# Optimization experiments

Hardware: AMD Instinct MI355X
Metric: run time of the kernel (lower is better)

Reference implementation:

```python
import jax, jax.numpy as jnp
import numpy as np

LN_EPS = 1e-12  # BERT default layer_norm_eps


def setup_inputs() -> dict:
    key = jax.random.key(0)
    ks = jax.random.split(key, 8)
    B, S, H, I, E = 4, 2048, 1024, 4096, 8
    sH = 1.0 / np.sqrt(H)
    sI = 1.0 / np.sqrt(I)
    return {
        "hidden_states": jax.random.normal(ks[0], (B, S, H), dtype=jnp.float32),
        "Wr": jax.random.uniform(ks[1], (E, H), jnp.float32, -sH, sH),      # router (no bias)
        "W1": jax.random.uniform(ks[2], (E, H, I), jnp.float32, -sH, sH),   # per-expert BertIntermediate
        "b1": jax.random.uniform(ks[3], (E, I), jnp.float32, -sH, sH),
        "Wo": jax.random.uniform(ks[4], (I, H), jnp.float32, -sI, sI),      # shared BertOutput dense
        "bo": jax.random.uniform(ks[5], (H,), jnp.float32, -sI, sI),
        "gamma": jnp.ones((H,), jnp.float32),
        "beta": jnp.zeros((H,), jnp.float32),
    }


def reference(hidden_states, Wr, W1, b1, Wo, bo, gamma, beta):
    B, S, H = hidden_states.shape
    E = Wr.shape[0]
    x = hidden_states.reshape(-1, H)                      # [N, H]
    router_logits = x @ Wr.T                              # [N, E]
    # top-1 expert per token (router probs are NOT used to scale outputs in the original)
    expert_idx = jnp.argmax(jax.nn.softmax(router_logits, axis=-1), axis=-1)  # [N]
    # dispatch == per-token expert FFN; accumulate masked per-expert outputs
    inter = jnp.zeros((x.shape[0], W1.shape[2]), dtype=x.dtype)  # [N, I]
    for e in range(E):  # fixed small expert count
        mask = (expert_idx == e)[:, None].astype(x.dtype)
        inter = inter + mask * jax.nn.gelu(x @ W1[e] + b1[e], approximate=False)
    # shared BertOutput: dense -> (dropout off) -> residual -> LayerNorm
    y = inter @ Wo + bo + x                               # [N, H]
    mu = jnp.mean(y, axis=-1, keepdims=True)
    var = jnp.mean(jnp.square(y - mu), axis=-1, keepdims=True)
    out = (y - mu) * jax.lax.rsqrt(var + LN_EPS) * gamma + beta
    return out.reshape(B, S, H)
```

## Files before the change

### kernel.cpp

```cpp
#include <hip/hip_runtime.h>
#include <hip/hip_bf16.h>
#include <math.h>

#define NTOK 8192
#define HD 1024
#define ID 4096
#define NE 8
#define MAXTILES 72
#define SORTT 512
#define TPT (NTOK / SORTT)

typedef __attribute__((ext_vector_type(8))) short short8;
typedef __attribute__((ext_vector_type(8))) unsigned short ushort8;
typedef __attribute__((ext_vector_type(4))) float floatx4;

__device__ __forceinline__ unsigned short f2bf(float f) {
  unsigned int u = __float_as_uint(f);
  return (unsigned short)((u + 0x7fffu + ((u >> 16) & 1u)) >> 16);
}

__device__ __forceinline__ void async_ld16(const void* g, void* l) {
  __builtin_amdgcn_global_load_lds(
      (const __attribute__((address_space(1))) unsigned int*)g,
      (__attribute__((address_space(3))) unsigned int*)l,
      16, 0, 0);
}


__global__ void transpose_cast_kernel(const float* __restrict__ src,
                                      unsigned short* __restrict__ dst, int R, int C) {
  size_t bo = (size_t)blockIdx.z * R * C;
  src += bo; dst += bo;
  __shared__ float t[64][65];
  int c0 = blockIdx.x * 64, r0 = blockIdx.y * 64;
  int tid = threadIdx.x;
  int rr = tid >> 4, c4 = (tid & 15) * 4;
#pragma unroll
  for (int q = 0; q < 4; q++) {
    int r = rr + q * 16;
    float4 v = *(const float4*)(src + (size_t)(r0 + r) * C + c0 + c4);
    t[r][c4] = v.x; t[r][c4 + 1] = v.y; t[r][c4 + 2] = v.z; t[r][c4 + 3] = v.w;
  }
  __syncthreads();
  int r8 = (tid & 7) * 8;
#pragma unroll
  for (int q = 0; q < 2; q++) {
    int cc = (tid >> 3) + q * 32;
    ushort8 o;
#pragma unroll
    for (int i = 0; i < 8; i++) o[i] = f2bf(t[r8 + i][cc]);
    *(ushort8*)(dst + (size_t)(c0 + cc) * R + r0 + r8) = o;
  }
}

__global__ void router_kernel(const float* __restrict__ x, const float* __restrict__ wr,
                              int* __restrict__ eidx, unsigned short* __restrict__ xb) {
  int wave = threadIdx.x >> 6, lane = threadIdx.x & 63;
  int n = blockIdx.x * 4 + wave;
  const float* xr = x + (size_t)n * HD;
  unsigned short* xbr = xb + (size_t)n * HD;
  double acc[NE];
#pragma unroll
  for (int e = 0; e < NE; e++) acc[e] = 0.0;
#pragma unroll
  for (int v = 0; v < 4; v++) {
    int h = (lane + v * 64) * 4;
    float4 xv = *(const float4*)(xr + h);
    ushort4 o;
    o.x = f2bf(xv.x); o.y = f2bf(xv.y); o.z = f2bf(xv.z); o.w = f2bf(xv.w);
    *(ushort4*)(xbr + h) = o;
#pragma unroll
    for (int e = 0; e < NE; e++) {
      float4 wv = *(const float4*)(wr + e * HD + h);
      acc[e] += (double)xv.x * wv.x + (double)xv.y * wv.y +
                (double)xv.z * wv.z + (double)xv.w * wv.w;
    }
  }
#pragma unroll
  for (int m = 32; m >= 1; m >>= 1) {
#pragma unroll
    for (int e = 0; e < NE; e++) acc[e] += __shfl_xor(acc[e], m, 64);
  }
  if (lane == 0) {
    int best = 0; double bv = acc[0];
#pragma unroll
    for (int e = 1; e < NE; e++) if (acc[e] > bv) { bv = acc[e]; best = e; }
    eidx[n] = best;
  }
}

__global__ __launch_bounds__(SORTT) void sort_kernel(
    const int* __restrict__ eidx, int* __restrict__ ntiles, int* __restrict__ tile_e,
    int* __restrict__ tile_base, int* __restrict__ tile_len, int* __restrict__ perm) {
  __shared__ int h[NE][SORTT];
  __shared__ int off_sh[NE];
  __shared__ int tot[NE];
  int t = threadIdx.x;
  int wave = t >> 6, lane = t & 63;
  const int base = t * TPT;

  int4 e0 = *(const int4*)(eidx + base);
  int4 e1 = *(const int4*)(eidx + base + 4);
  int4 e2 = *(const int4*)(eidx + base + 8);
  int4 e3 = *(const int4*)(eidx + base + 12);
  int ex[TPT] = {e0.x, e0.y, e0.z, e0.w, e1.x, e1.y, e1.z, e1.w,
                 e2.x, e2.y, e2.z, e2.w, e3.x, e3.y, e3.z, e3.w};
  int cnt0 = 0, cnt1 = 0, cnt2 = 0, cnt3 = 0, cnt4 = 0, cnt5 = 0, cnt6 = 0, cnt7 = 0;
#pragma unroll
  for (int i = 0; i < TPT; i++) {
    int e = ex[i];
    cnt0 += (e == 0); cnt1 += (e == 1); cnt2 += (e == 2); cnt3 += (e == 3);
    cnt4 += (e == 4); cnt5 += (e == 5); cnt6 += (e == 6); cnt7 += (e == 7);
  }
  h[0][t] = cnt0; h[1][t] = cnt1; h[2][t] = cnt2; h[3][t] = cnt3;
  h[4][t] = cnt4; h[5][t] = cnt5; h[6][t] = cnt6; h[7][t] = cnt7;
  __syncthreads();

  {
    int e = wave;
    int v[8], s = 0;
#pragma unroll
    for (int i = 0; i < 8; i++) { v[i] = h[e][lane * 8 + i]; s += v[i]; }
    int inc = s;
#pragma unroll
    for (int d = 1; d < 64; d <<= 1) {
      int o = __shfl_up(inc, d, 64);
      if (lane >= d) inc += o;
    }
    int exc = inc - s;
#pragma unroll
    for (int i = 0; i < 8; i++) { h[e][lane * 8 + i] = exc; exc += v[i]; }
    if (lane == 63) tot[e] = inc;
  }
  __syncthreads();

  if (t == 0) {
    int s = 0, tt = 0;
    for (int e = 0; e < NE; e++) {
      off_sh[e] = s;
      int c = tot[e];
      for (int b = 0; b < c; b += 128) {
        tile_e[tt] = e;
        tile_base[tt] = s + b;
        tile_len[tt] = (c - b < 128) ? (c - b) : 128;
        tt++;
      }
      s += c;
    }
    *ntiles = tt;
  }
  __syncthreads();

  int c0c = off_sh[0] + h[0][t], c1c = off_sh[1] + h[1][t];
  int c2c = off_sh[2] + h[2][t], c3c = off_sh[3] + h[3][t];
  int c4c = off_sh[4] + h[4][t], c5c = off_sh[5] + h[5][t];
  int c6c = off_sh[6] + h[6][t], c7c = off_sh[7] + h[7][t];
#pragma unroll
  for (int i = 0; i < TPT; i++) {
    int e = ex[i];
    int pos = c0c;
    pos = (e == 1) ? c1c : pos; pos = (e == 2) ? c2c : pos;
    pos = (e == 3) ? c3c : pos; pos = (e == 4) ? c4c : pos;
    pos = (e == 5) ? c5c : pos; pos = (e == 6) ? c6c : pos;
    pos = (e == 7) ? c7c : pos;
    perm[pos] = base + i;
    c0c += (e == 0); c1c += (e == 1); c2c += (e == 2); c3c += (e == 3);
    c4c += (e == 4); c5c += (e == 5); c6c += (e == 6); c7c += (e == 7);
  }
}


__global__ __launch_bounds__(256, 2) void ffn1_kernel(
    const unsigned short* __restrict__ xb, const unsigned short* __restrict__ w1t,
    const float* __restrict__ b1, const int* __restrict__ perm,
    const int* __restrict__ ntiles, const int* __restrict__ tile_e,
    const int* __restrict__ tile_base, const int* __restrict__ tile_len,
    unsigned short* __restrict__ interb) {
  int t = blockIdx.y;
  if (t >= *ntiles) return;
  int e = tile_e[t], base = tile_base[t], len = tile_len[t];
  int nb = blockIdx.x * 128;

  __shared__ unsigned short lA[128 * 64];
  __shared__ unsigned short lB[128 * 64];

  int tid = threadIdx.x;
  int wave = tid >> 6, lane = tid & 63;
  int lr = lane >> 3;
  int chunk = (lane & 7) ^ lr;

  const unsigned short* gA[4];
  const unsigned short* gB[4];
#pragma unroll
  for (int q = 0; q < 4; q++) {
    int c = wave * 4 + q;
    int tr = c * 8 + lr;
    int token = perm[base + (tr < len ? tr : len - 1)];
    gA[q] = xb + (size_t)token * HD + chunk * 8;
    int nr = nb + c * 8 + lr;
    gB[q] = w1t + ((size_t)e * ID + nr) * HD + chunk * 8;
  }

  floatx4 acc[4][4];
#pragma unroll
  for (int i = 0; i < 4; i++)
#pragma unroll
    for (int j = 0; j < 4; j++) acc[i][j] = (floatx4){0.f, 0.f, 0.f, 0.f};

  int wm = (wave >> 1) * 64, wn = (wave & 1) * 64;
  int c15 = lane & 15, q4 = lane >> 4;

  for (int ko = 0; ko < HD / 64; ko++) {
#pragma unroll
    for (int q = 0; q < 4; q++) {
      int c = wave * 4 + q;
      async_ld16(gA[q] + ko * 64, &lA[c * 512]);
      async_ld16(gB[q] + ko * 64, &lB[c * 512]);
    }
    __syncthreads();
#pragma unroll
    for (int kk = 0; kk < 2; kk++) {
      short8 af[4], bfr[4];
#pragma unroll
      for (int i = 0; i < 4; i++) {
        int m = wm + i * 16 + c15;
        int sa = (kk * 4 + q4) ^ (m & 7);
        af[i] = *(const short8*)&lA[m * 64 + sa * 8];
        int n = wn + i * 16 + c15;
        int sb = (kk * 4 + q4) ^ (n & 7);
        bfr[i] = *(const short8*)&lB[n * 64 + sb * 8];
      }
#pragma unroll
      for (int i = 0; i < 4; i++)
#pragma unroll
        for (int j = 0; j < 4; j++)
          acc[i][j] = __builtin_amdgcn_mfma_f32_16x16x32_bf16(af[i], bfr[j], acc[i][j], 0, 0, 0);
    }
    __syncthreads();
  }

#pragma unroll
  for (int i = 0; i < 4; i++) {
#pragma unroll
    for (int r = 0; r < 4; r++) {
      int tr = wm + i * 16 + q4 * 4 + r;
      if (tr >= len) continue;
      int token = perm[base + tr];
#pragma unroll
      for (int j = 0; j < 4; j++) {
        int col = nb + wn + j * 16 + c15;
        float v = acc[i][j][r] + b1[e * ID + col];
        v = 0.5f * v * (1.0f + erff(v * 0.70710678118654752f));
        interb[(size_t)token * ID + col] = f2bf(v);
      }
    }
  }
}

__global__ __launch_bounds__(256, 2) void ffn2_kernel(
    const unsigned short* __restrict__ interb, const unsigned short* __restrict__ wot,
    const float* __restrict__ bo, const float* __restrict__ x, float* __restrict__ y) {
  int tm = blockIdx.y;
  int nb = blockIdx.x * 128;

  __shared__ unsigned short lA[128 * 64];
  __shared__ unsigned short lB[128 * 64];

  int tid = threadIdx.x;
  int wave = tid >> 6, lane = tid & 63;
  int lr = lane >> 3;
  int chunk = (lane & 7) ^ lr;

  const unsigned short* gA[4];
  const unsigned short* gB[4];
#pragma unroll
  for (int q = 0; q < 4; q++) {
    int c = wave * 4 + q;
    int row = tm * 128 + c * 8 + lr;
    gA[q] = interb + (size_t)row * ID + chunk * 8;
    int nr = nb + c * 8 + lr;
    gB[q] = wot + (size_t)nr * ID + chunk * 8;
  }

  floatx4 acc[4][4];
#pragma unroll
  for (int i = 0; i < 4; i++)
#pragma unroll
    for (int j = 0; j < 4; j++) acc[i][j] = (floatx4){0.f, 0.f, 0.f, 0.f};

  int wm = (wave >> 1) * 64, wn = (wave & 1) * 64;
  int c15 = lane & 15, q4 = lane >> 4;

  for (int ko = 0; ko < ID / 64; ko++) {
#pragma unroll
    for (int q = 0; q < 4; q++) {
      int c = wave * 4 + q;
      async_ld16(gA[q] + ko * 64, &lA[c * 512]);
      async_ld16(gB[q] + ko * 64, &lB[c * 512]);
    }
    __syncthreads();
#pragma unroll
    for (int kk = 0; kk < 2; kk++) {
      short8 af[4], bfr[4];
#pragma unroll
      for (int i = 0; i < 4; i++) {
        int m = wm + i * 16 + c15;
        int sa = (kk * 4 + q4) ^ (m & 7);
        af[i] = *(const short8*)&lA[m * 64 + sa * 8];
        int n = wn + i * 16 + c15;
        int sb = (kk * 4 + q4) ^ (n & 7);
        bfr[i] = *(const short8*)&lB[n * 64 + sb * 8];
      }
#pragma unroll
      for (int i = 0; i < 4; i++)
#pragma unroll
        for (int j = 0; j < 4; j++)
          acc[i][j] = __builtin_amdgcn_mfma_f32_16x16x32_bf16(af[i], bfr[j], acc[i][j], 0, 0, 0);
    }
    __syncthreads();
  }

#pragma unroll
  for (int i = 0; i < 4; i++) {
#pragma unroll
    for (int r = 0; r < 4; r++) {
      int row = tm * 128 + wm + i * 16 + q4 * 4 + r;
#pragma unroll
      for (int j = 0; j < 4; j++) {
        int col = nb + wn + j * 16 + c15;
        float v = acc[i][j][r] + bo[col] + x[(size_t)row * HD + col];
        y[(size_t)row * HD + col] = v;
      }
    }
  }
}

__global__ void ln_kernel(float* __restrict__ y, const float* __restrict__ gamma,
                          const float* __restrict__ beta) {
  int row = blockIdx.x, t = threadIdx.x;
  int lane = t & 63, wave = t >> 6;
  float* yr = y + (size_t)row * HD;
  float4 v = *(const float4*)(yr + t * 4);
  float s = v.x + v.y + v.z + v.w;
  float ss = v.x * v.x + v.y * v.y + v.z * v.z + v.w * v.w;
#pragma unroll
  for (int m = 32; m >= 1; m >>= 1) {
    s += __shfl_xor(s, m, 64);
    ss += __shfl_xor(ss, m, 64);
  }
  __shared__ float sred[4], ssred[4];
  if (lane == 0) { sred[wave] = s; ssred[wave] = ss; }
  __syncthreads();
  s = sred[0] + sred[1] + sred[2] + sred[3];
  ss = ssred[0] + ssred[1] + ssred[2] + ssred[3];
  float mu = s * (1.0f / HD);
  float var = ss * (1.0f / HD) - mu * mu;
  float rs = rsqrtf(var + 1e-12f);
  float4 g = *(const float4*)(gamma + t * 4);
  float4 b = *(const float4*)(beta + t * 4);
  float4 o;
  o.x = (v.x - mu) * rs * g.x + b.x;
  o.y = (v.y - mu) * rs * g.y + b.y;
  o.z = (v.z - mu) * rs * g.z + b.z;
  o.w = (v.w - mu) * rs * g.w + b.w;
  *(float4*)(yr + t * 4) = o;
}


extern "C" void kernel_launch(void* const* d_in, const int* in_sizes, int n_in,
                              void* d_out, int out_size, void* d_ws, size_t ws_size,
                              hipStream_t stream) {
  const float* x     = (const float*)d_in[0];
  const float* wr    = (const float*)d_in[1];
  const float* w1    = (const float*)d_in[2];
  const float* b1    = (const float*)d_in[3];
  const float* wo    = (const float*)d_in[4];
  const float* bo    = (const float*)d_in[5];
  const float* gamma = (const float*)d_in[6];
  const float* beta  = (const float*)d_in[7];
  float* out = (float*)d_out;

  char* p = (char*)d_ws;
  unsigned short* w1t = (unsigned short*)p; p += (size_t)NE * ID * HD * 2;
  unsigned short* wot = (unsigned short*)p; p += (size_t)HD * ID * 2;
  unsigned short* xb  = (unsigned short*)p; p += (size_t)NTOK * HD * 2;
  unsigned short* interb = (unsigned short*)p; p += (size_t)NTOK * ID * 2;
  int* eidx = (int*)p; p += (size_t)NTOK * 4;
  int* perm = (int*)p; p += (size_t)NTOK * 4;
  int* ints = (int*)p;
  int* ntiles    = ints;
  int* tile_e    = ints + 8;
  int* tile_base = ints + 80;
  int* tile_len  = ints + 152;

  router_kernel<<<NTOK / 4, 256, 0, stream>>>(x, wr, eidx, xb);
  transpose_cast_kernel<<<dim3(ID / 64, HD / 64, NE), 256, 0, stream>>>(w1, w1t, HD, ID);
  transpose_cast_kernel<<<dim3(HD / 64, ID / 64, 1), 256, 0, stream>>>(wo, wot, ID, HD);
  sort_kernel<<<1, SORTT, 0, stream>>>(eidx, ntiles, tile_e, tile_base, tile_len, perm);
  ffn1_kernel<<<dim3(ID / 128, MAXTILES), 256, 0, stream>>>(
      xb, w1t, b1, perm, ntiles, tile_e, tile_base, tile_len, interb);
  ffn2_kernel<<<dim3(HD / 128, NTOK / 128), 256, 0, stream>>>(interb, wot, bo, x, out);
  ln_kernel<<<NTOK, 256, 0, stream>>>(out, gamma, beta);
}
```

Before: 500.2 us.

## Double-buffer LDS tiles in both expert GEMM kernels to overlap loads

Both the expert FFN1 and shared FFN2 GEMM kernels get two LDS buffers per operand. The tile for the next K step is issued with async global-to-LDS loads before the MFMA work on the current tile. This removes the pre-compute barrier that left matrix cores idle during each global load. In exchange, LDS use per block doubles to 64 KB, which could limit occupancy, and correctness relies on the end-of-iteration barrier waiting for the outstanding async loads.

```diff
diff --git a/kernel.cpp b/kernel.cpp
--- a/kernel.cpp
+++ b/kernel.cpp
@@ -170,6 +170,8 @@
 }
 
 
+#define LBUF (128 * 64)
+
 __global__ __launch_bounds__(256, 2) void ffn1_kernel(
     const unsigned short* __restrict__ xb, const unsigned short* __restrict__ w1t,
     const float* __restrict__ b1, const int* __restrict__ perm,
@@ -181,8 +183,8 @@
   int e = tile_e[t], base = tile_base[t], len = tile_len[t];
   int nb = blockIdx.x * 128;
 
-  __shared__ unsigned short lA[128 * 64];
-  __shared__ unsigned short lB[128 * 64];
+  __shared__ unsigned short lA[2 * LBUF];
+  __shared__ unsigned short lB[2 * LBUF];
 
   int tid = threadIdx.x;
   int wave = tid >> 6, lane = tid & 63;
@@ -210,14 +212,26 @@
   int wm = (wave >> 1) * 64, wn = (wave & 1) * 64;
   int c15 = lane & 15, q4 = lane >> 4;
 
-  for (int ko = 0; ko < HD / 64; ko++) {
-#pragma unroll
-    for (int q = 0; q < 4; q++) {
-      int c = wave * 4 + q;
-      async_ld16(gA[q] + ko * 64, &lA[c * 512]);
-      async_ld16(gB[q] + ko * 64, &lB[c * 512]);
-    }
-    __syncthreads();
+  const int NK = HD / 64;
+#pragma unroll
+  for (int q = 0; q < 4; q++) {
+    int c = wave * 4 + q;
+    async_ld16(gA[q], &lA[c * 512]);
+    async_ld16(gB[q], &lB[c * 512]);
+  }
+  __syncthreads();
+
+  for (int ko = 0; ko < NK; ko++) {
+    int cur = (ko & 1) * LBUF;
+    int nxt = (cur ^ LBUF);
+    if (ko + 1 < NK) {
+#pragma unroll
+      for (int q = 0; q < 4; q++) {
+        int c = wave * 4 + q;
+        async_ld16(gA[q] + (ko + 1) * 64, &lA[nxt + c * 512]);
+        async_ld16(gB[q] + (ko + 1) * 64, &lB[nxt + c * 512]);
+      }
+    }
 #pragma unroll
     for (int kk = 0; kk < 2; kk++) {
       short8 af[4], bfr[4];
@@ -225,10 +239,10 @@
       for (int i = 0; i < 4; i++) {
         int m = wm + i * 16 + c15;
         int sa = (kk * 4 + q4) ^ (m & 7);
-        af[i] = *(const short8*)&lA[m * 64 + sa * 8];
+        af[i] = *(const short8*)&lA[cur + m * 64 + sa * 8];
         int n = wn + i * 16 + c15;
         int sb = (kk * 4 + q4) ^ (n & 7);
-        bfr[i] = *(const short8*)&lB[n * 64 + sb * 8];
+        bfr[i] = *(const short8*)&lB[cur + n * 64 + sb * 8];
       }
 #pragma unroll
       for (int i = 0; i < 4; i++)
@@ -263,8 +277,8 @@
   int tm = blockIdx.y;
   int nb = blockIdx.x * 128;
 
-  __shared__ unsigned short lA[128 * 64];
-  __shared__ unsigned short lB[128 * 64];
+  __shared__ unsigned short lA[2 * LBUF];
+  __shared__ unsigned short lB[2 * LBUF];
 
   int tid = threadIdx.x;
   int wave = tid >> 6, lane = tid & 63;
@@ -291,14 +305,26 @@
   int wm = (wave >> 1) * 64, wn = (wave & 1) * 64;
   int c15 = lane & 15, q4 = lane >> 4;
 
-  for (int ko = 0; ko < ID / 64; ko++) {
-#pragma unroll
-    for (int q = 0; q < 4; q++) {
-      int c = wave * 4 + q;
-      async_ld16(gA[q] + ko * 64, &lA[c * 512]);
-      async_ld16(gB[q] + ko * 64, &lB[c * 512]);
-    }
-    __syncthreads();
+  const int NK = ID / 64;
+#pragma unroll
+  for (int q = 0; q < 4; q++) {
+    int c = wave * 4 + q;
+    async_ld16(gA[q], &lA[c * 512]);
+    async_ld16(gB[q], &lB[c * 512]);
+  }
+  __syncthreads();
+
+  for (int ko = 0; ko < NK; ko++) {
+    int cur = (ko & 1) * LBUF;
+    int nxt = (cur ^ LBUF);
+    if (ko + 1 < NK) {
+#pragma unroll
+      for (int q = 0; q < 4; q++) {
+        int c = wave * 4 + q;
+        async_ld16(gA[q] + (ko + 1) * 64, &lA[nxt + c * 512]);
+        async_ld16(gB[q] + (ko + 1) * 64, &lB[nxt + c * 512]);
+      }
+    }
 #pragma unroll
     for (int kk = 0; kk < 2; kk++) {
       short8 af[4], bfr[4];
@@ -306,10 +332,10 @@
       for (int i = 0; i < 4; i++) {
         int m = wm + i * 16 + c15;
         int sa = (kk * 4 + q4) ^ (m & 7);
-        af[i] = *(const short8*)&lA[m * 64 + sa * 8];
+        af[i] = *(const short8*)&lA[cur + m * 64 + sa * 8];
         int n = wn + i * 16 + c15;
         int sb = (kk * 4 + q4) ^ (n & 7);
-        bfr[i] = *(const short8*)&lB[n * 64 + sb * 8];
+        bfr[i] = *(const short8*)&lB[cur + n * 64 + sb * 8];
       }
 #pragma unroll
       for (int i = 0; i < 4; i++)
```

Result: slower. 547.3 us (+9.4%).

## Use 256x256 tiles with double-buffered 8-phase async pipeline in FFN GEMMs

Applied to the files above, without the earlier changes.

Both expert and output GEMMs move from 128x128 tiles with 4 waves and a single LDS buffer to 256x256 tiles with 8 waves. Global-to-LDS async loads are double-buffered and interleaved across eight MFMA phases using explicit vmcnt waits, barriers and setprio. Expert tiles in the sort kernel grow to 256 tokens, with MAXTILES reduced to 40. The aim is to hide load latency and raise arithmetic intensity. The cost is 128KB of LDS per block, which may limit occupancy, and more padding waste on partial expert tiles.

```diff
diff --git a/kernel.cpp b/kernel.cpp
--- a/kernel.cpp
+++ b/kernel.cpp
@@ -6,7 +6,7 @@
 #define HD 1024
 #define ID 4096
 #define NE 8
-#define MAXTILES 72
+#define MAXTILES 40
 #define SORTT 512
 #define TPT (NTOK / SORTT)
 
@@ -139,10 +139,10 @@
     for (int e = 0; e < NE; e++) {
       off_sh[e] = s;
       int c = tot[e];
-      for (int b = 0; b < c; b += 128) {
+      for (int b = 0; b < c; b += 256) {
         tile_e[tt] = e;
         tile_base[tt] = s + b;
-        tile_len[tt] = (c - b < 128) ? (c - b) : 128;
+        tile_len[tt] = (c - b < 256) ? (c - b) : 256;
         tt++;
       }
       s += c;
@@ -170,7 +170,91 @@
 }
 
 
-__global__ __launch_bounds__(256, 2) void ffn1_kernel(
+#define VMC6() asm volatile("s_waitcnt vmcnt(6)" ::: "memory")
+#define VMC0() asm volatile("s_waitcnt vmcnt(0)" ::: "memory")
+#define NOPS ((void)0)
+
+#define SA8(BUF, kt, q) \
+  async_ld16(gAq[q] + (size_t)(kt) * 64, lA + ((BUF) * 16384 + ((q) * 64 + wave * 8) * 64))
+#define SB8(BUF, kt, q) \
+  async_ld16(gBq[q] + (size_t)(kt) * 64, lB + ((BUF) * 16384 + ((q) * 64 + wave * 8) * 64))
+
+#define MF4(AV, KK, I)                                                                       \
+  acc[I][0] = __builtin_amdgcn_mfma_f32_16x16x32_bf16(AV, bf[0][KK], acc[I][0], 0, 0, 0);    \
+  acc[I][1] = __builtin_amdgcn_mfma_f32_16x16x32_bf16(AV, bf[1][KK], acc[I][1], 0, 0, 0);    \
+  acc[I][2] = __builtin_amdgcn_mfma_f32_16x16x32_bf16(AV, bf[2][KK], acc[I][2], 0, 0, 0);    \
+  acc[I][3] = __builtin_amdgcn_mfma_f32_16x16x32_bf16(AV, bf[3][KK], acc[I][3], 0, 0, 0);
+
+#define PH8(BT, I, STG, TAIL)                                                  \
+  {                                                                            \
+    short8 a0k0 = *(const short8*)(lA + (BT) * 16384 + aoff[I] + sx0);         \
+    short8 a0k1 = *(const short8*)(lA + (BT) * 16384 + aoff[I] + sx1);         \
+    short8 a1k0 = *(const short8*)(lA + (BT) * 16384 + aoff[(I) + 1] + sx0);   \
+    short8 a1k1 = *(const short8*)(lA + (BT) * 16384 + aoff[(I) + 1] + sx1);   \
+    STG;                                                                       \
+    __builtin_amdgcn_s_barrier();                                              \
+    __builtin_amdgcn_s_setprio(1);                                             \
+    MF4(a0k0, 0, I) MF4(a0k1, 1, I)                                            \
+    MF4(a1k0, 0, (I) + 1) MF4(a1k1, 1, (I) + 1)                                \
+    __builtin_amdgcn_s_setprio(0);                                             \
+    TAIL;                                                                      \
+    __builtin_amdgcn_s_barrier();                                              \
+  }
+
+#define LOADB8(BT)                                                             \
+  bf[0][0] = *(const short8*)(lB + (BT) * 16384 + boff[0] + sx0);              \
+  bf[0][1] = *(const short8*)(lB + (BT) * 16384 + boff[0] + sx1);              \
+  bf[1][0] = *(const short8*)(lB + (BT) * 16384 + boff[1] + sx0);              \
+  bf[1][1] = *(const short8*)(lB + (BT) * 16384 + boff[1] + sx1);              \
+  bf[2][0] = *(const short8*)(lB + (BT) * 16384 + boff[2] + sx0);              \
+  bf[2][1] = *(const short8*)(lB + (BT) * 16384 + boff[2] + sx1);              \
+  bf[3][0] = *(const short8*)(lB + (BT) * 16384 + boff[3] + sx0);              \
+  bf[3][1] = *(const short8*)(lB + (BT) * 16384 + boff[3] + sx1);
+
+template <int NK>
+__device__ __forceinline__ void gemm8phase(const unsigned short* const* gAq,
+                                           const unsigned short* const* gBq,
+                                           unsigned short* lA, unsigned short* lB,
+                                           int wave, int lane, floatx4 (&acc)[8][4]) {
+  int c15 = lane & 15, q4 = lane >> 4, c7 = c15 & 7;
+  int wm = wave >> 2, wn = wave & 3;
+  int sx0 = (q4 ^ c7) * 8;
+  int sx1 = ((4 + q4) ^ c7) * 8;
+  int aoff[8], boff[4];
+#pragma unroll
+  for (int i = 0; i < 8; i++) aoff[i] = (wm * 128 + i * 16 + c15) * 64;
+#pragma unroll
+  for (int j = 0; j < 4; j++) boff[j] = (wn * 64 + j * 16 + c15) * 64;
+
+  SB8(0, 0, 0); SB8(0, 0, 1); SB8(0, 0, 2); SB8(0, 0, 3);
+  SA8(0, 0, 0); SA8(0, 0, 2); SA8(0, 0, 1); SA8(0, 0, 3);
+  SB8(1, 1, 0); SB8(1, 1, 1); SB8(1, 1, 2); SB8(1, 1, 3);
+  SA8(1, 1, 0); SA8(1, 1, 2);
+  VMC6();
+  __builtin_amdgcn_s_barrier();
+
+  short8 bf[4][2];
+#pragma unroll 1
+  for (int u = 0; u < NK / 2; ++u) {
+    int kt0 = 2 * u;
+    bool last = (u == NK / 2 - 1);
+    LOADB8(0)
+    PH8(0, 0, SA8(1, kt0 + 1, 1); SA8(1, kt0 + 1, 3), NOPS)
+    PH8(0, 2, if (!last) { SB8(0, kt0 + 2, 0); SB8(0, kt0 + 2, 1); }, NOPS)
+    PH8(0, 4, if (!last) { SB8(0, kt0 + 2, 2); SB8(0, kt0 + 2, 3); }, NOPS)
+    PH8(0, 6, if (!last) { SA8(0, kt0 + 2, 0); SA8(0, kt0 + 2, 2); },
+        if (last) VMC0(); else VMC6())
+    LOADB8(1)
+    PH8(1, 0, if (!last) { SA8(0, kt0 + 2, 1); SA8(0, kt0 + 2, 3); }, NOPS)
+    PH8(1, 2, if (!last) { SB8(1, kt0 + 3, 0); SB8(1, kt0 + 3, 1); }, NOPS)
+    PH8(1, 4, if (!last) { SB8(1, kt0 + 3, 2); SB8(1, kt0 + 3, 3); }, NOPS)
+    PH8(1, 6, if (!last) { SA8(1, kt0 + 3, 0); SA8(1, kt0 + 3, 2); },
+        if (!last) VMC6())
+  }
+}
+
+
+__global__ __launch_bounds__(512, 2) void ffn1_kernel(
     const unsigned short* __restrict__ xb, const unsigned short* __restrict__ w1t,
     const float* __restrict__ b1, const int* __restrict__ perm,
     const int* __restrict__ ntiles, const int* __restrict__ tile_e,
@@ -179,76 +263,46 @@
   int t = blockIdx.y;
   if (t >= *ntiles) return;
   int e = tile_e[t], base = tile_base[t], len = tile_len[t];
-  int nb = blockIdx.x * 128;
-
-  __shared__ unsigned short lA[128 * 64];
-  __shared__ unsigned short lB[128 * 64];
+  int nb = blockIdx.x * 256;
+
+  __shared__ unsigned short lA[2 * 16384];
+  __shared__ unsigned short lB[2 * 16384];
 
   int tid = threadIdx.x;
   int wave = tid >> 6, lane = tid & 63;
-  int lr = lane >> 3;
-  int chunk = (lane & 7) ^ lr;
-
-  const unsigned short* gA[4];
-  const unsigned short* gB[4];
+  int lr = lane >> 3, l7 = lane & 7;
+  int chunk = l7 ^ lr;
+
+  const unsigned short* gAq[4];
+  const unsigned short* gBq[4];
 #pragma unroll
   for (int q = 0; q < 4; q++) {
-    int c = wave * 4 + q;
-    int tr = c * 8 + lr;
-    int token = perm[base + (tr < len ? tr : len - 1)];
-    gA[q] = xb + (size_t)token * HD + chunk * 8;
-    int nr = nb + c * 8 + lr;
-    gB[q] = w1t + ((size_t)e * ID + nr) * HD + chunk * 8;
-  }
-
-  floatx4 acc[4][4];
-#pragma unroll
-  for (int i = 0; i < 4; i++)
+    int rr = q * 64 + wave * 8 + lr;
+    int token = perm[base + (rr < len ? rr : len - 1)];
+    gAq[q] = xb + (size_t)token * HD + chunk * 8;
+    gBq[q] = w1t + ((size_t)e * ID + nb + rr) * HD + chunk * 8;
+  }
+
+  floatx4 acc[8][4];
+#pragma unroll
+  for (int i = 0; i < 8; i++)
 #pragma unroll
     for (int j = 0; j < 4; j++) acc[i][j] = (floatx4){0.f, 0.f, 0.f, 0.f};
 
-  int wm = (wave >> 1) * 64, wn = (wave & 1) * 64;
+  gemm8phase<HD / 64>(gAq, gBq, lA, lB, wave, lane, acc);
+
   int c15 = lane & 15, q4 = lane >> 4;
-
-  for (int ko = 0; ko < HD / 64; ko++) {
-#pragma unroll
-    for (int q = 0; q < 4; q++) {
-      int c = wave * 4 + q;
-      async_ld16(gA[q] + ko * 64, &lA[c * 512]);
-      async_ld16(gB[q] + ko * 64, &lB[c * 512]);
-    }
-    __syncthreads();
-#pragma unroll
-    for (int kk = 0; kk < 2; kk++) {
-      short8 af[4], bfr[4];
-#pragma unroll
-      for (int i = 0; i < 4; i++) {
-        int m = wm + i * 16 + c15;
-        int sa = (kk * 4 + q4) ^ (m & 7);
-        af[i] = *(const short8*)&lA[m * 64 + sa * 8];
-        int n = wn + i * 16 + c15;
-        int sb = (kk * 4 + q4) ^ (n & 7);
-        bfr[i] = *(const short8*)&lB[n * 64 + sb * 8];
-      }
-#pragma unroll
-      for (int i = 0; i < 4; i++)
-#pragma unroll
-        for (int j = 0; j < 4; j++)
-          acc[i][j] = __builtin_amdgcn_mfma_f32_16x16x32_bf16(af[i], bfr[j], acc[i][j], 0, 0, 0);
-    }
-    __syncthreads();
-  }
-
-#pragma unroll
-  for (int i = 0; i < 4; i++) {
+  int wm = wave >> 2, wn = wave & 3;
+#pragma unroll
+  for (int i = 0; i < 8; i++) {
 #pragma unroll
     for (int r = 0; r < 4; r++) {
-      int tr = wm + i * 16 + q4 * 4 + r;
+      int tr = wm * 128 + i * 16 + q4 * 4 + r;
       if (tr >= len) continue;
       int token = perm[base + tr];
 #pragma unroll
       for (int j = 0; j < 4; j++) {
-        int col = nb + wn + j * 16 + c15;
+        int col = nb + wn * 64 + j * 16 + c15;
         float v = acc[i][j][r] + b1[e * ID + col];
         v = 0.5f * v * (1.0f + erff(v * 0.70710678118654752f));
         interb[(size_t)token * ID + col] = f2bf(v);
@@ -257,77 +311,47 @@
   }
 }
 
-__global__ __launch_bounds__(256, 2) void ffn2_kernel(
+__global__ __launch_bounds__(512, 2) void ffn2_kernel(
     const unsigned short* __restrict__ interb, const unsigned short* __restrict__ wot,
     const float* __restrict__ bo, const float* __restrict__ x, float* __restrict__ y) {
   int tm = blockIdx.y;
-  int nb = blockIdx.x * 128;
-
-  __shared__ unsigned short lA[128 * 64];
-  __shared__ unsigned short lB[128 * 64];
+  int nb = blockIdx.x * 256;
+
+  __shared__ unsigned short lA[2 * 16384];
+  __shared__ unsigned short lB[2 * 16384];
 
   int tid = threadIdx.x;
   int wave = tid >> 6, lane = tid & 63;
-  int lr = lane >> 3;
-  int chunk = (lane & 7) ^ lr;
-
-  const unsigned short* gA[4];
-  const unsigned short* gB[4];
+  int lr = lane >> 3, l7 = lane & 7;
+  int chunk = l7 ^ lr;
+
+  const unsigned short* gAq[4];
+  const unsigned short* gBq[4];
 #pragma unroll
   for (int q = 0; q < 4; q++) {
-    int c = wave * 4 + q;
-    int row = tm * 128 + c * 8 + lr;
-    gA[q] = interb + (size_t)row * ID + chunk * 8;
-    int nr = nb + c * 8 + lr;
-    gB[q] = wot + (size_t)nr * ID + chunk * 8;
-  }
-
-  floatx4 acc[4][4];
-#pragma unroll
-  for (int i = 0; i < 4; i++)
+    int rr = q * 64 + wave * 8 + lr;
+    gAq[q] = interb + (size_t)(tm * 256 + rr) * ID + chunk * 8;
+    gBq[q] = wot + (size_t)(nb + rr) * ID + chunk * 8;
+  }
+
+  floatx4 acc[8][4];
+#pragma unroll
+  for (int i = 0; i < 8; i++)
 #pragma unroll
     for (int j = 0; j < 4; j++) acc[i][j] = (floatx4){0.f, 0.f, 0.f, 0.f};
 
-  int wm = (wave >> 1) * 64, wn = (wave & 1) * 64;
+  gemm8phase<ID / 64>(gAq, gBq, lA, lB, wave, lane, acc);
+
   int c15 = lane & 15, q4 = lane >> 4;
-
-  for (int ko = 0; ko < ID / 64; ko++) {
-#pragma unroll
-    for (int q = 0; q < 4; q++) {
-      int c = wave * 4 + q;
-      async_ld16(gA[q] + ko * 64, &lA[c * 512]);
-      async_ld16(gB[q] + ko * 64, &lB[c * 512]);
-    }
-    __syncthreads();
-#pragma unroll
-    for (int kk = 0; kk < 2; kk++) {
-      short8 af[4], bfr[4];
-#pragma unroll
-      for (int i = 0; i < 4; i++) {
-        int m = wm + i * 16 + c15;
-        int sa = (kk * 4 + q4) ^ (m & 7);
-        af[i] = *(const short8*)&lA[m * 64 + sa * 8];
-        int n = wn + i * 16 + c15;
-        int sb = (kk * 4 + q4) ^ (n & 7);
-        bfr[i] = *(const short8*)&lB[n * 64 + sb * 8];
-      }
-#pragma unroll
-      for (int i = 0; i < 4; i++)
-#pragma unroll
-        for (int j = 0; j < 4; j++)
-          acc[i][j] = __builtin_amdgcn_mfma_f32_16x16x32_bf16(af[i], bfr[j], acc[i][j], 0, 0, 0);
-    }
-    __syncthreads();
-  }
-
-#pragma unroll
-  for (int i = 0; i < 4; i++) {
+  int wm = wave >> 2, wn = wave & 3;
+#pragma unroll
+  for (int i = 0; i < 8; i++) {
 #pragma unroll
     for (int r = 0; r < 4; r++) {
-      int row = tm * 128 + wm + i * 16 + q4 * 4 + r;
+      int row = tm * 256 + wm * 128 + i * 16 + q4 * 4 + r;
 #pragma unroll
       for (int j = 0; j < 4; j++) {
-        int col = nb + wn + j * 16 + c15;
+        int col = nb + wn * 64 + j * 16 + c15;
         float v = acc[i][j][r] + bo[col] + x[(size_t)row * HD + col];
         y[(size_t)row * HD + col] = v;
       }
@@ -397,8 +421,8 @@
   transpose_cast_kernel<<<dim3(ID / 64, HD / 64, NE), 256, 0, stream>>>(w1, w1t, HD, ID);
   transpose_cast_kernel<<<dim3(HD / 64, ID / 64, 1), 256, 0, stream>>>(wo, wot, ID, HD);
   sort_kernel<<<1, SORTT, 0, stream>>>(eidx, ntiles, tile_e, tile_base, tile_len, perm);
-  ffn1_kernel<<<dim3(ID / 128, MAXTILES), 256, 0, stream>>>(
+  ffn1_kernel<<<dim3(ID / 256, MAXTILES), 512, 0, stream>>>(
       xb, w1t, b1, perm, ntiles, tile_e, tile_base, tile_len, interb);
-  ffn2_kernel<<<dim3(HD / 128, NTOK / 128), 256, 0, stream>>>(interb, wot, bo, x, out);
+  ffn2_kernel<<<dim3(HD / 256, NTOK / 256), 512, 0, stream>>>(interb, wot, bo, x, out);
   ln_kernel<<<NTOK, 256, 0, stream>>>(out, gamma, beta);
 }
```

Result: slower. 570.1 us (+14.0%).

## Fuse preamble kernels and remap GEMM block indices for XCD-aware L2 reuse

Applied to the files above, without the earlier changes.

Merges the router and the two weight transpose-cast launches into one preamble kernel that dispatches on block index, which removes launch gaps and tail effects between them. Both FFN GEMMs now use a flattened 1D grid with a swizzled block-to-tile mapping. The mapping uses the low 3 bits, likely matching the round-robin dispatch across the 8 XCDs, so blocks sharing A rows or B columns land on the same XCD and reuse its L2. The risk is that the remap assumes a specific dispatch order, and mixing different work types in one grid can unbalance the preamble.

```diff
diff --git a/kernel.cpp b/kernel.cpp
--- a/kernel.cpp
+++ b/kernel.cpp
@@ -27,12 +27,13 @@
 }
 
 
-__global__ void transpose_cast_kernel(const float* __restrict__ src,
-                                      unsigned short* __restrict__ dst, int R, int C) {
-  size_t bo = (size_t)blockIdx.z * R * C;
+__device__ __forceinline__ void transpose_tile(const float* __restrict__ src,
+                                               unsigned short* __restrict__ dst,
+                                               int R, int C, int bx, int by, int bz,
+                                               float (*t)[65]) {
+  size_t bo = (size_t)bz * R * C;
   src += bo; dst += bo;
-  __shared__ float t[64][65];
-  int c0 = blockIdx.x * 64, r0 = blockIdx.y * 64;
+  int c0 = bx * 64, r0 = by * 64;
   int tid = threadIdx.x;
   int rr = tid >> 4, c4 = (tid & 15) * 4;
 #pragma unroll
@@ -53,10 +54,12 @@
   }
 }
 
-__global__ void router_kernel(const float* __restrict__ x, const float* __restrict__ wr,
-                              int* __restrict__ eidx, unsigned short* __restrict__ xb) {
+__device__ __forceinline__ void router_body(const float* __restrict__ x,
+                                            const float* __restrict__ wr,
+                                            int* __restrict__ eidx,
+                                            unsigned short* __restrict__ xb, int nbase) {
   int wave = threadIdx.x >> 6, lane = threadIdx.x & 63;
-  int n = blockIdx.x * 4 + wave;
+  int n = nbase + wave;
   const float* xr = x + (size_t)n * HD;
   unsigned short* xbr = xb + (size_t)n * HD;
   double acc[NE];
@@ -86,6 +89,22 @@
 #pragma unroll
     for (int e = 1; e < NE; e++) if (acc[e] > bv) { bv = acc[e]; best = e; }
     eidx[n] = best;
+  }
+}
+
+__global__ void preamble_kernel(const float* __restrict__ x, const float* __restrict__ wr,
+                                const float* __restrict__ w1, const float* __restrict__ wo,
+                                unsigned short* __restrict__ w1t, unsigned short* __restrict__ wot,
+                                int* __restrict__ eidx, unsigned short* __restrict__ xb) {
+  __shared__ float tile[64][65];
+  int b = blockIdx.x;
+  if (b < 8192) {
+    transpose_tile(w1, w1t, HD, ID, b & 63, (b >> 6) & 15, b >> 10, tile);
+  } else if (b < 9216) {
+    int bb = b - 8192;
+    transpose_tile(wo, wot, ID, HD, bb & 15, bb >> 4, 0, tile);
+  } else {
+    router_body(x, wr, eidx, xb, (b - 9216) * 4);
   }
 }
 
@@ -176,10 +195,13 @@
     const int* __restrict__ ntiles, const int* __restrict__ tile_e,
     const int* __restrict__ tile_base, const int* __restrict__ tile_len,
     unsigned short* __restrict__ interb) {
-  int t = blockIdx.y;
+  int w = blockIdx.x;
+  int x = w & 7, s = w >> 3;
+  int hh = x & 1, q = x >> 1;
+  int t = q * 18 + (s >> 4);
   if (t >= *ntiles) return;
+  int nb = (hh * 16 + (s & 15)) * 128;
   int e = tile_e[t], base = tile_base[t], len = tile_len[t];
-  int nb = blockIdx.x * 128;
 
   __shared__ unsigned short lA[128 * 64];
   __shared__ unsigned short lB[128 * 64];
@@ -192,13 +214,13 @@
   const unsigned short* gA[4];
   const unsigned short* gB[4];
 #pragma unroll
-  for (int q = 0; q < 4; q++) {
-    int c = wave * 4 + q;
+  for (int qq = 0; qq < 4; qq++) {
+    int c = wave * 4 + qq;
     int tr = c * 8 + lr;
     int token = perm[base + (tr < len ? tr : len - 1)];
-    gA[q] = xb + (size_t)token * HD + chunk * 8;
+    gA[qq] = xb + (size_t)token * HD + chunk * 8;
     int nr = nb + c * 8 + lr;
-    gB[q] = w1t + ((size_t)e * ID + nr) * HD + chunk * 8;
+    gB[qq] = w1t + ((size_t)e * ID + nr) * HD + chunk * 8;
   }
 
   floatx4 acc[4][4];
@@ -212,10 +234,10 @@
 
   for (int ko = 0; ko < HD / 64; ko++) {
 #pragma unroll
-    for (int q = 0; q < 4; q++) {
-      int c = wave * 4 + q;
-      async_ld16(gA[q] + ko * 64, &lA[c * 512]);
-      async_ld16(gB[q] + ko * 64, &lB[c * 512]);
+    for (int qq = 0; qq < 4; qq++) {
+      int c = wave * 4 + qq;
+      async_ld16(gA[qq] + ko * 64, &lA[c * 512]);
+      async_ld16(gB[qq] + ko * 64, &lB[c * 512]);
     }
     __syncthreads();
 #pragma unroll
@@ -260,8 +282,11 @@
 __global__ __launch_bounds__(256, 2) void ffn2_kernel(
     const unsigned short* __restrict__ interb, const unsigned short* __restrict__ wot,
     const float* __restrict__ bo, const float* __restrict__ x, float* __restrict__ y) {
-  int tm = blockIdx.y;
-  int nb = blockIdx.x * 128;
+  int w = blockIdx.x;
+  int x8 = w & 7, s = w >> 3;
+  int mq = x8 >> 1, nh = x8 & 1;
+  int tm = mq * 16 + (s >> 2);
+  int nb = (nh * 4 + (s & 3)) * 128;
 
   __shared__ unsigned short lA[128 * 64];
   __shared__ unsigned short lB[128 * 64];
@@ -274,12 +299,12 @@
   const unsigned short* gA[4];
   const unsigned short* gB[4];
 #pragma unroll
-  for (int q = 0; q < 4; q++) {
-    int c = wave * 4 + q;
+  for (int qq = 0; qq < 4; qq++) {
+    int c = wave * 4 + qq;
     int row = tm * 128 + c * 8 + lr;
-    gA[q] = interb + (size_t)row * ID + chunk * 8;
+    gA[qq] = interb + (size_t)row * ID + chunk * 8;
     int nr = nb + c * 8 + lr;
-    gB[q] = wot + (size_t)nr * ID + chunk * 8;
+    gB[qq] = wot + (size_t)nr * ID + chunk * 8;
   }
 
   floatx4 acc[4][4];
@@ -293,10 +318,10 @@
 
   for (int ko = 0; ko < ID / 64; ko++) {
 #pragma unroll
-    for (int q = 0; q < 4; q++) {
-      int c = wave * 4 + q;
-      async_ld16(gA[q] + ko * 64, &lA[c * 512]);
-      async_ld16(gB[q] + ko * 64, &lB[c * 512]);
+    for (int qq = 0; qq < 4; qq++) {
+      int c = wave * 4 + qq;
+      async_ld16(gA[qq] + ko * 64, &lA[c * 512]);
+      async_ld16(gB[qq] + ko * 64, &lB[c * 512]);
     }
     __syncthreads();
 #pragma unroll
@@ -393,12 +418,10 @@
   int* tile_base = ints + 80;
   int* tile_len  = ints + 152;
 
-  router_kernel<<<NTOK / 4, 256, 0, stream>>>(x, wr, eidx, xb);
-  transpose_cast_kernel<<<dim3(ID / 64, HD / 64, NE), 256, 0, stream>>>(w1, w1t, HD, ID);
-  transpose_cast_kernel<<<dim3(HD / 64, ID / 64, 1), 256, 0, stream>>>(wo, wot, ID, HD);
+  preamble_kernel<<<11264, 256, 0, stream>>>(x, wr, w1, wo, w1t, wot, eidx, xb);
   sort_kernel<<<1, SORTT, 0, stream>>>(eidx, ntiles, tile_e, tile_base, tile_len, perm);
-  ffn1_kernel<<<dim3(ID / 128, MAXTILES), 256, 0, stream>>>(
+  ffn1_kernel<<<2304, 256, 0, stream>>>(
       xb, w1t, b1, perm, ntiles, tile_e, tile_base, tile_len, interb);
-  ffn2_kernel<<<dim3(HD / 128, NTOK / 128), 256, 0, stream>>>(interb, wot, bo, x, out);
+  ffn2_kernel<<<512, 256, 0, stream>>>(interb, wot, bo, x, out);
   ln_kernel<<<NTOK, 256, 0, stream>>>(out, gamma, beta);
 }
```

Result: faster. 474.3 us (-5.2%).
